# Kernel optimization log

Hardware: AMD Instinct MI355X
Metric: run time of the kernel (lower is better)

The kernel has to match this reference:

```python
import jax, jax.numpy as jnp
import numpy as np

T, IN_DIM, HID, OUT = 32768, 500, 300, 100


def setup_inputs() -> dict:
    key = jax.random.key(0)
    ks = jax.random.split(key, 12)
    s_in = 1.0 / np.sqrt(HID)
    inp = {
        'input_seq': jax.random.normal(ks[0], (T, IN_DIM), jnp.float32),
        'W_ih0': jax.random.uniform(ks[1], (HID, IN_DIM), jnp.float32, -s_in, s_in),
        'W_hh0': jax.random.uniform(ks[2], (HID, HID), jnp.float32, -s_in, s_in),
        'b_ih0': jax.random.uniform(ks[3], (HID,), jnp.float32, -s_in, s_in),
        'b_hh0': jax.random.uniform(ks[4], (HID,), jnp.float32, -s_in, s_in),
        'W_ih1': jax.random.uniform(ks[5], (HID, HID), jnp.float32, -s_in, s_in),
        'W_hh1': jax.random.uniform(ks[6], (HID, HID), jnp.float32, -s_in, s_in),
        'b_ih1': jax.random.uniform(ks[7], (HID,), jnp.float32, -s_in, s_in),
        'b_hh1': jax.random.uniform(ks[8], (HID,), jnp.float32, -s_in, s_in),
        'W_lin': jax.random.uniform(ks[9], (OUT, HID), jnp.float32, -s_in, s_in),
        'b_lin': jax.random.uniform(ks[10], (OUT,), jnp.float32, -s_in, s_in),
    }
    return inp


def _rnn_layer(x_proj, W_hh):
    # x_proj: [T, H] = precomputed input projection + both biases
    # h_t = tanh(x_proj_t + h_{t-1} @ W_hh^T), h_0 = 0 (PyTorch nn.RNN semantics)
    def step(h, xp):
        h_new = jnp.tanh(xp + h @ W_hh.T)
        return h_new, h_new
    h0 = jnp.zeros((W_hh.shape[0],), x_proj.dtype)
    _, hs = jax.lax.scan(step, h0, x_proj)
    return hs  # [T, H]


def reference(input_seq, W_ih0, W_hh0, b_ih0, b_hh0, W_ih1, W_hh1, b_ih1, b_hh1, W_lin, b_lin):
    # Layer 0: batch-1 vanilla tanh RNN; vectorize input GEMM over all timesteps
    x0 = input_seq @ W_ih0.T + (b_ih0 + b_hh0)  # [T, HID]
    h0 = _rnn_layer(x0, W_hh0)
    # Layer 1 consumes layer-0 hidden sequence
    x1 = h0 @ W_ih1.T + (b_ih1 + b_hh1)  # [T, HID]
    h1 = _rnn_layer(x1, W_hh1)
    # Linear head over flattened [T, HID]
    return h1 @ W_lin.T + b_lin  # [T, OUT]
```

## Files before the change

kernel.cpp:

```cpp
#include <hip/hip_runtime.h>
#include <cstddef>

#define T_LEN 32768
#define HID   300
#define HP    304
#define HK    320
#define KC    10
#define IN_D  500
#define OUT_D 100
#define OUTP  104
#define DIST  2
#define CHUNK 64
#define NCHUNK (T_LEN / CHUNK)

typedef _Float16 f16x8 __attribute__((ext_vector_type(8)));
typedef float    f32x4 __attribute__((ext_vector_type(4)));

__device__ __align__(16) float    g_x  [(size_t)(T_LEN + 8) * HP];
__device__ __align__(16) float    g_x1 [(size_t)(T_LEN + 8) * HP];
__device__ __align__(16) _Float16 g_h0h[(size_t)T_LEN * HP + 64];
__device__ __align__(16) _Float16 g_h1h[(size_t)T_LEN * HP + 64];
__device__ __align__(16) float    g_wt0[IN_D * HP];
__device__ __align__(16) float    g_wtl[HID * OUTP];
__device__ int g_flag0;
__device__ int g_flag1;

__global__ void k_reset() { g_flag0 = 0; g_flag1 = 0; }

__global__ void k_transpose(const float* __restrict__ src, int J, int K, int JP, int dst_sel)
{
    float* dst = (dst_sel == 0) ? g_wt0 : g_wtl;
    int idx = blockIdx.x * 256 + threadIdx.x;
    if (idx >= K * JP) return;
    int k = idx / JP, j = idx - k * JP;
    dst[idx] = (j < J) ? src[j * K + k] : 0.f;
}

__global__ __launch_bounds__(320) void k_gemm_in(const float* __restrict__ inp,
                                                 const float* __restrict__ b1,
                                                 const float* __restrict__ b2)
{
    __shared__ float lds[32 * IN_D];
    const int tid = threadIdx.x;
    const int t0  = blockIdx.x * 32;
    {
        const f32x4* src4 = (const f32x4*)(inp + (size_t)t0 * IN_D);
        f32x4* lds4 = (f32x4*)lds;
        const int n4 = (32 * IN_D) >> 2;
        for (int i = tid; i < n4; i += 320) lds4[i] = src4[i];
    }
    __syncthreads();
    const int j = tid;
    if (j >= HP) return;
    float acc[32];
#pragma unroll
    for (int i = 0; i < 32; i++) acc[i] = 0.f;
#pragma unroll 4
    for (int k = 0; k < IN_D; k++) {
        float w = g_wt0[k * HP + j];
#pragma unroll
        for (int i = 0; i < 32; i++) acc[i] += w * lds[i * IN_D + k];
    }
    const float bias = (j < HID) ? (b1[j] + b2[j]) : 0.f;
#pragma unroll 4
    for (int i = 0; i < 32; i++) g_x[(size_t)(t0 + i) * HP + j] = acc[i] + bias;
}

__global__ __launch_bounds__(128) void k_gemm_out(const float* __restrict__ blin,
                                                  float* __restrict__ out)
{
    __shared__ float lds[64 * HP];
    const int tid = threadIdx.x;
    const int t0  = blockIdx.x * 64;
    {
        const f16x8* src8 = (const f16x8*)(g_h1h + (size_t)t0 * HP);
        const int n8 = (64 * HP) / 8;
        for (int i = tid; i < n8; i += 128) {
            f16x8 v = src8[i];
            float* d = &lds[i * 8];
#pragma unroll
            for (int e = 0; e < 8; e++) d[e] = (float)v[e];
        }
    }
    __syncthreads();
    const int j = tid;
    if (j >= OUTP) return;
    float acc[64];
#pragma unroll
    for (int i = 0; i < 64; i++) acc[i] = 0.f;
#pragma unroll 2
    for (int k = 0; k < HID; k++) {
        float w = g_wtl[k * OUTP + j];
#pragma unroll
        for (int i = 0; i < 64; i++) acc[i] += w * lds[i * HP + k];
    }
    if (j < OUT_D) {
        float b = blin[j];
        for (int i = 0; i < 64; i++) out[(size_t)(t0 + i) * OUT_D + j] = acc[i] + b;
    }
}

__device__ __forceinline__ float fast_tanh(float v)
{
    float e = __expf(2.f * v);
    return 1.f - 2.f * __builtin_amdgcn_rcpf(e + 1.f);
}

__device__ __forceinline__ float sel4(f32x4 a, bool c1, bool c2)
{
    float v01 = c1 ? a[1] : a[0];
    float v23 = c1 ? a[3] : a[2];
    return c2 ? v23 : v01;
}

__device__ __forceinline__ f16x8 loadw_frag(const float* __restrict__ W,
                                            int tile, int col, int g, int kc)
{
    const int row = tile * 16 + col;
    const int kb  = kc * 32 + g * 8;
    f16x8 f;
#pragma unroll
    for (int j = 0; j < 8; j++) {
        const int k = kb + j;
        float wv = (row < HID && k < HID) ? W[row * HID + k] : 0.f;
        f[j] = (_Float16)wv;
    }
    return f;
}

__device__ __forceinline__ void wait_flag(int* f, int target)
{
    if (threadIdx.x == 0) {
        while (__hip_atomic_load(f, __ATOMIC_ACQUIRE, __HIP_MEMORY_SCOPE_AGENT) < target)
            __builtin_amdgcn_s_sleep(8);
    }
    __syncthreads();
}

__device__ __forceinline__ void publish_flag(int* f, int v)
{
    __syncthreads();
    if (threadIdx.x == 0)
        __hip_atomic_store(f, v, __ATOMIC_RELEASE, __HIP_MEMORY_SCOPE_AGENT);
}

#define MF(a_, b_, c_) __builtin_amdgcn_mfma_f32_16x16x32_f16((a_), (b_), (c_), 0, 0, 0)

template<int ROLE0>
__device__ __forceinline__ void scan_role(_Float16 (*hlds)[HK],
                                          const float* __restrict__ Whh,
                                          const float* __restrict__ xin,
                                          _Float16* __restrict__ hseq)
{
    const int tid  = threadIdx.x;
    const int lane = tid & 63;
    const int wave = tid >> 6;
    const int col  = lane & 15;
    const int g    = lane >> 4;
    const bool c1  = (col & 1) != 0;
    const bool c2  = (col & 2) != 0;
    const bool writer = (col < 4);

    const int tA = wave, tB = wave + 8, tC = wave + 16;
    const bool hasC = (wave < 3);
    const int wbA = tA * 16 + g * 4;
    const int wbB = tB * 16 + g * 4;
    const int wbC = tC * 16 + g * 4;

    for (int i = tid; i < 2 * HK; i += 512) ((_Float16*)hlds)[i] = (_Float16)0.f;

    f16x8 wA[KC], wB[KC], wC[KC];
#pragma unroll
    for (int kc = 0; kc < KC; kc++) {
        wA[kc] = loadw_frag(Whh, tA, col, g, kc);
        wB[kc] = loadw_frag(Whh, tB, col, g, kc);
        if (hasC) wC[kc] = loadw_frag(Whh, tC, col, g, kc);
        else {
            f16x8 z;
#pragma unroll
            for (int j = 0; j < 8; j++) z[j] = (_Float16)0.f;
            wC[kc] = z;
        }
    }

    __syncthreads();

    if (!ROLE0) wait_flag(&g_flag1, NCHUNK < 2 ? NCHUNK : 2);

    const f32x4 Z = {0.f, 0.f, 0.f, 0.f};

    f32x4 xA[DIST], xB[DIST], xC[DIST];
#pragma unroll
    for (int s = 0; s < DIST; s++) {
        xA[s] = *(const f32x4*)&xin[(size_t)s * HP + wbA];
        xB[s] = *(const f32x4*)&xin[(size_t)s * HP + wbB];
        xC[s] = hasC ? *(const f32x4*)&xin[(size_t)s * HP + wbC] : Z;
    }

#define STEP(t_, R_, s_) do {                                                          \
        f16x8 bf[KC];                                                                  \
        _Pragma("unroll")                                                              \
        for (int kc = 0; kc < KC; kc++)                                                \
            bf[kc] = *(const f16x8*)&hlds[R_][kc * 32 + g * 8];                        \
        f32x4 xvA = xA[s_], xvB = xB[s_], xvC = xC[s_];                                \
        xA[s_] = *(const f32x4*)&xin[(size_t)((t_) + DIST) * HP + wbA];                \
        xB[s_] = *(const f32x4*)&xin[(size_t)((t_) + DIST) * HP + wbB];                \
        if (hasC) xC[s_] = *(const f32x4*)&xin[(size_t)((t_) + DIST) * HP + wbC];      \
                                            \
        f32x4 cA0 = MF(wA[0], bf[0], xvA), cB0 = MF(wB[0], bf[0], xvB);                \
        f32x4 cC0 = hasC ? MF(wC[0], bf[0], xvC) : Z;                                  \
        f32x4 cA1 = MF(wA[3], bf[3], Z),   cB1 = MF(wB[3], bf[3], Z);                  \
        f32x4 cC1 = hasC ? MF(wC[3], bf[3], Z) : Z;                                    \
        f32x4 cA2 = MF(wA[6], bf[6], Z),   cB2 = MF(wB[6], bf[6], Z);                  \
        f32x4 cC2 = hasC ? MF(wC[6], bf[6], Z) : Z;                                    \
        f32x4 cA3 = MF(wA[8], bf[8], Z),   cB3 = MF(wB[8], bf[8], Z);                  \
        f32x4 cC3 = hasC ? MF(wC[8], bf[8], Z) : Z;                                    \
                                                                          \
        cA0 = MF(wA[1], bf[1], cA0); cB0 = MF(wB[1], bf[1], cB0);                      \
        if (hasC) cC0 = MF(wC[1], bf[1], cC0);                                         \
        cA1 = MF(wA[4], bf[4], cA1); cB1 = MF(wB[4], bf[4], cB1);                      \
        if (hasC) cC1 = MF(wC[4], bf[4], cC1);                                         \
        cA2 = MF(wA[7], bf[7], cA2); cB2 = MF(wB[7], bf[7], cB2);                      \
        if (hasC) cC2 = MF(wC[7], bf[7], cC2);                                         \
        cA3 = MF(wA[9], bf[9], cA3); cB3 = MF(wB[9], bf[9], cB3);                      \
        if (hasC) cC3 = MF(wC[9], bf[9], cC3);                                         \
                                                        \
        cA0 = MF(wA[2], bf[2], cA0); cB0 = MF(wB[2], bf[2], cB0);                      \
        if (hasC) cC0 = MF(wC[2], bf[2], cC0);                                         \
        cA1 = MF(wA[5], bf[5], cA1); cB1 = MF(wB[5], bf[5], cB1);                      \
        if (hasC) cC1 = MF(wC[5], bf[5], cC1);                                         \
                                                              \
        f32x4 sumA = (cA0 + cA1) + (cA2 + cA3);                                        \
        f32x4 sumB = (cB0 + cB1) + (cB2 + cB3);                                        \
        float yA = fast_tanh(sel4(sumA, c1, c2));                                      \
        float yB = fast_tanh(sel4(sumB, c1, c2));                                      \
        float yC = 0.f;                                                                \
        if (hasC) {                                                                    \
            f32x4 sumC = (cC0 + cC1) + (cC2 + cC3);                                    \
            yC = fast_tanh(sel4(sumC, c1, c2));                                        \
        }                                                                              \
        if (writer) {                                                                  \
            _Float16 hA = (_Float16)yA, hB = (_Float16)yB, hC = (_Float16)yC;          \
            hlds[1 - (R_)][wbA + col] = hA;                                            \
            hlds[1 - (R_)][wbB + col] = hB;                                            \
            if (hasC) hlds[1 - (R_)][wbC + col] = hC;                                  \
            hseq[(size_t)(t_) * HP + wbA + col] = hA;                                  \
            hseq[(size_t)(t_) * HP + wbB + col] = hB;                                  \
            if (hasC) hseq[(size_t)(t_) * HP + wbC + col] = hC;                        \
        }                                                                              \
    } while (0)

#define BAR() asm volatile("s_waitcnt lgkmcnt(0)\n\ts_barrier" ::: "memory")

#pragma unroll 1
    for (int c = 0; c < NCHUNK; ++c) {
        if (!ROLE0 && c > 0) {
            int tgt = (c + 2) < NCHUNK ? (c + 2) : NCHUNK;
            wait_flag(&g_flag1, tgt);
        }
#pragma unroll 1
        for (int tt = 0; tt < CHUNK; tt += 2) {
            const int tb = c * CHUNK + tt;
            STEP(tb + 0, 0, 0); BAR();
            STEP(tb + 1, 1, 1); BAR();
        }
        if (ROLE0) publish_flag(&g_flag0, c + 1);
    }
#undef STEP
#undef BAR
}

__device__ __forceinline__ void proj_role(const float* __restrict__ Wih,
                                          const float* __restrict__ b1,
                                          const float* __restrict__ b2)
{
    const int tid  = threadIdx.x;
    const int lane = tid & 63;
    const int wave = tid >> 6;
    const int col  = lane & 15;
    const int g    = lane >> 4;

    const int tA = wave, tB = wave + 8, tC = wave + 16;
    const bool hasC = (wave < 3);

    f16x8 wA[KC], wB[KC], wC[KC];
#pragma unroll
    for (int kc = 0; kc < KC; kc++) {
        wA[kc] = loadw_frag(Wih, tA, col, g, kc);
        wB[kc] = loadw_frag(Wih, tB, col, g, kc);
        if (hasC) wC[kc] = loadw_frag(Wih, tC, col, g, kc);
        else {
            f16x8 z;
#pragma unroll
            for (int j = 0; j < 8; j++) z[j] = (_Float16)0.f;
            wC[kc] = z;
        }
    }
    f32x4 bA, bB, bC;
#pragma unroll
    for (int e = 0; e < 4; e++) {
        int jA = tA * 16 + g * 4 + e, jB = tB * 16 + g * 4 + e, jC = tC * 16 + g * 4 + e;
        bA[e] = (jA < HID) ? b1[jA] + b2[jA] : 0.f;
        bB[e] = (jB < HID) ? b1[jB] + b2[jB] : 0.f;
        bC[e] = (hasC && jC < HID) ? b1[jC] + b2[jC] : 0.f;
    }

    const f32x4 zero4 = {0.f, 0.f, 0.f, 0.f};

#pragma unroll 1
    for (int c = 0; c < NCHUNK; ++c) {
        wait_flag(&g_flag0, c + 1);
        const int tbase = c * CHUNK;
#pragma unroll
        for (int tg = 0; tg < 4; ++tg) {
            const int t = tbase + tg * 16 + col;
            f16x8 bf[KC];
#pragma unroll
            for (int kc = 0; kc < KC; ++kc)
                bf[kc] = *(const f16x8*)&g_h0h[(size_t)t * HP + kc * 32 + g * 8];
            f32x4 aA = zero4, aB = zero4, aC = zero4;
#pragma unroll
            for (int kc = 0; kc < KC; ++kc) {
                aA = MF(wA[kc], bf[kc], aA);
                aB = MF(wB[kc], bf[kc], aB);
                if (hasC) aC = MF(wC[kc], bf[kc], aC);
            }
            *(f32x4*)&g_x1[(size_t)t * HP + tA * 16 + g * 4] = aA + bA;
            *(f32x4*)&g_x1[(size_t)t * HP + tB * 16 + g * 4] = aB + bB;
            if (hasC)
            *(f32x4*)&g_x1[(size_t)t * HP + tC * 16 + g * 4] = aC + bC;
        }
        publish_flag(&g_flag1, c + 1);
    }
}

__global__ __launch_bounds__(512, 2) void k_pipeline(const float* __restrict__ W_hh0,
                                                     const float* __restrict__ W_ih1,
                                                     const float* __restrict__ b_ih1,
                                                     const float* __restrict__ b_hh1,
                                                     const float* __restrict__ W_hh1)
{
    __shared__ __align__(16) _Float16 hlds[2][HK];
    if (blockIdx.x == 0)
        scan_role<1>(hlds, W_hh0, g_x, g_h0h);
    else if (blockIdx.x == 1)
        proj_role(W_ih1, b_ih1, b_hh1);
    else
        scan_role<0>(hlds, W_hh1, g_x1, g_h1h);
}

extern "C" void kernel_launch(void* const* d_in, const int* in_sizes, int n_in,
                              void* d_out, int out_size, void* d_ws, size_t ws_size,
                              hipStream_t stream)
{
    (void)in_sizes; (void)n_in; (void)d_ws; (void)ws_size; (void)out_size;
    const float* input = (const float*)d_in[0];
    const float* W_ih0 = (const float*)d_in[1];
    const float* W_hh0 = (const float*)d_in[2];
    const float* b_ih0 = (const float*)d_in[3];
    const float* b_hh0 = (const float*)d_in[4];
    const float* W_ih1 = (const float*)d_in[5];
    const float* W_hh1 = (const float*)d_in[6];
    const float* b_ih1 = (const float*)d_in[7];
    const float* b_hh1 = (const float*)d_in[8];
    const float* W_lin = (const float*)d_in[9];
    const float* b_lin = (const float*)d_in[10];
    float* out = (float*)d_out;

    k_reset<<<dim3(1), dim3(1), 0, stream>>>();
    k_transpose<<<dim3((IN_D * HP + 255) / 256), dim3(256), 0, stream>>>(W_ih0, HID, IN_D, HP, 0);
    k_transpose<<<dim3((HID * OUTP + 255) / 256), dim3(256), 0, stream>>>(W_lin, OUT_D, HID, OUTP, 2);

    k_gemm_in<<<dim3(T_LEN / 32), dim3(320), 0, stream>>>(input, b_ih0, b_hh0);

    k_pipeline<<<dim3(3), dim3(512), 0, stream>>>(W_hh0, W_ih1, b_ih1, b_hh1, W_hh1);

    k_gemm_out<<<dim3(T_LEN / 64), dim3(128), 0, stream>>>(b_lin, out);
}
```

Measured before the change: 26.04 ms.

## Spread recurrent scan over 12 waves with two tiles each and deeper prefetch

Raises the pipeline block from 8 to 12 waves, so each wave owns at most two 16-row output tiles of the 19 instead of three. This shortens the serial MFMA chain per timestep. Each lane now loads one scalar x value per tile, added after the MFMA reduction instead of being used as the accumulator init. The prefetch distance goes from 2 to 4 and the step loop is unrolled by 4. The trade-off is more waves joining each per-step barrier and higher block-level register pressure under the new launch bounds.

```diff
diff --git a/kernel.cpp b/kernel.cpp
--- a/kernel.cpp
+++ b/kernel.cpp
@@ -9,9 +9,10 @@
 #define IN_D  500
 #define OUT_D 100
 #define OUTP  104
-#define DIST  2
+#define DIST  4
 #define CHUNK 64
 #define NCHUNK (T_LEN / CHUNK)
+#define NWAVE 12
 
 typedef _Float16 f16x8 __attribute__((ext_vector_type(8)));
 typedef float    f32x4 __attribute__((ext_vector_type(4)));
@@ -157,29 +158,28 @@
     const int wave = tid >> 6;
     const int col  = lane & 15;
     const int g    = lane >> 4;
+    const int rr   = col & 3;
     const bool c1  = (col & 1) != 0;
     const bool c2  = (col & 2) != 0;
     const bool writer = (col < 4);
 
-    const int tA = wave, tB = wave + 8, tC = wave + 16;
-    const bool hasC = (wave < 3);
-    const int wbA = tA * 16 + g * 4;
-    const int wbB = tB * 16 + g * 4;
-    const int wbC = tC * 16 + g * 4;
-
-    for (int i = tid; i < 2 * HK; i += 512) ((_Float16*)hlds)[i] = (_Float16)0.f;
-
-    f16x8 wA[KC], wB[KC], wC[KC];
+    const int tA = wave, tB = wave + NWAVE;
+    const bool hasB = (wave < 7);
+    const int rowA = tA * 16 + g * 4 + rr;
+    const int rowB = tB * 16 + g * 4 + rr;
+
+    for (int i = tid; i < 2 * HK; i += 64 * NWAVE) ((_Float16*)hlds)[i] = (_Float16)0.f;
+
+    f16x8 wA[KC], wB[KC];
 #pragma unroll
     for (int kc = 0; kc < KC; kc++) {
         wA[kc] = loadw_frag(Whh, tA, col, g, kc);
-        wB[kc] = loadw_frag(Whh, tB, col, g, kc);
-        if (hasC) wC[kc] = loadw_frag(Whh, tC, col, g, kc);
+        if (hasB) wB[kc] = loadw_frag(Whh, tB, col, g, kc);
         else {
             f16x8 z;
 #pragma unroll
             for (int j = 0; j < 8; j++) z[j] = (_Float16)0.f;
-            wC[kc] = z;
+            wB[kc] = z;
         }
     }
 
@@ -187,66 +187,47 @@
 
     if (!ROLE0) wait_flag(&g_flag1, NCHUNK < 2 ? NCHUNK : 2);
 
+    float xA[DIST], xB[DIST];
+#pragma unroll
+    for (int s = 0; s < DIST; s++) {
+        xA[s] = xin[(size_t)s * HP + rowA];
+        xB[s] = hasB ? xin[(size_t)s * HP + rowB] : 0.f;
+    }
+
     const f32x4 Z = {0.f, 0.f, 0.f, 0.f};
-
-    f32x4 xA[DIST], xB[DIST], xC[DIST];
-#pragma unroll
-    for (int s = 0; s < DIST; s++) {
-        xA[s] = *(const f32x4*)&xin[(size_t)s * HP + wbA];
-        xB[s] = *(const f32x4*)&xin[(size_t)s * HP + wbB];
-        xC[s] = hasC ? *(const f32x4*)&xin[(size_t)s * HP + wbC] : Z;
-    }
 
 #define STEP(t_, R_, s_) do {                                                          \
         f16x8 bf[KC];                                                                  \
         _Pragma("unroll")                                                              \
         for (int kc = 0; kc < KC; kc++)                                                \
             bf[kc] = *(const f16x8*)&hlds[R_][kc * 32 + g * 8];                        \
-        f32x4 xvA = xA[s_], xvB = xB[s_], xvC = xC[s_];                                \
-        xA[s_] = *(const f32x4*)&xin[(size_t)((t_) + DIST) * HP + wbA];                \
-        xB[s_] = *(const f32x4*)&xin[(size_t)((t_) + DIST) * HP + wbB];                \
-        if (hasC) xC[s_] = *(const f32x4*)&xin[(size_t)((t_) + DIST) * HP + wbC];      \
-                                            \
-        f32x4 cA0 = MF(wA[0], bf[0], xvA), cB0 = MF(wB[0], bf[0], xvB);                \
-        f32x4 cC0 = hasC ? MF(wC[0], bf[0], xvC) : Z;                                  \
-        f32x4 cA1 = MF(wA[3], bf[3], Z),   cB1 = MF(wB[3], bf[3], Z);                  \
-        f32x4 cC1 = hasC ? MF(wC[3], bf[3], Z) : Z;                                    \
-        f32x4 cA2 = MF(wA[6], bf[6], Z),   cB2 = MF(wB[6], bf[6], Z);                  \
-        f32x4 cC2 = hasC ? MF(wC[6], bf[6], Z) : Z;                                    \
-        f32x4 cA3 = MF(wA[8], bf[8], Z),   cB3 = MF(wB[8], bf[8], Z);                  \
-        f32x4 cC3 = hasC ? MF(wC[8], bf[8], Z) : Z;                                    \
-                                                                          \
-        cA0 = MF(wA[1], bf[1], cA0); cB0 = MF(wB[1], bf[1], cB0);                      \
-        if (hasC) cC0 = MF(wC[1], bf[1], cC0);                                         \
-        cA1 = MF(wA[4], bf[4], cA1); cB1 = MF(wB[4], bf[4], cB1);                      \
-        if (hasC) cC1 = MF(wC[4], bf[4], cC1);                                         \
-        cA2 = MF(wA[7], bf[7], cA2); cB2 = MF(wB[7], bf[7], cB2);                      \
-        if (hasC) cC2 = MF(wC[7], bf[7], cC2);                                         \
-        cA3 = MF(wA[9], bf[9], cA3); cB3 = MF(wB[9], bf[9], cB3);                      \
-        if (hasC) cC3 = MF(wC[9], bf[9], cC3);                                         \
-                                                        \
-        cA0 = MF(wA[2], bf[2], cA0); cB0 = MF(wB[2], bf[2], cB0);                      \
-        if (hasC) cC0 = MF(wC[2], bf[2], cC0);                                         \
-        cA1 = MF(wA[5], bf[5], cA1); cB1 = MF(wB[5], bf[5], cB1);                      \
-        if (hasC) cC1 = MF(wC[5], bf[5], cC1);                                         \
-                                                              \
-        f32x4 sumA = (cA0 + cA1) + (cA2 + cA3);                                        \
-        f32x4 sumB = (cB0 + cB1) + (cB2 + cB3);                                        \
-        float yA = fast_tanh(sel4(sumA, c1, c2));                                      \
-        float yB = fast_tanh(sel4(sumB, c1, c2));                                      \
-        float yC = 0.f;                                                                \
-        if (hasC) {                                                                    \
-            f32x4 sumC = (cC0 + cC1) + (cC2 + cC3);                                    \
-            yC = fast_tanh(sel4(sumC, c1, c2));                                        \
+        float xvA = xA[s_], xvB = xB[s_];                                              \
+        xA[s_] = xin[(size_t)((t_) + DIST) * HP + rowA];                               \
+        if (hasB) xB[s_] = xin[(size_t)((t_) + DIST) * HP + rowB];                     \
+        f32x4 aA0 = MF(wA[0], bf[0], Z);                                               \
+        f32x4 aB0 = hasB ? MF(wB[0], bf[0], Z) : Z;                                    \
+        f32x4 aA1 = MF(wA[5], bf[5], Z);                                               \
+        f32x4 aB1 = hasB ? MF(wB[5], bf[5], Z) : Z;                                    \
+        _Pragma("unroll")                                                              \
+        for (int j = 1; j < 5; j++) {                                                  \
+            aA0 = MF(wA[j], bf[j], aA0);                                               \
+            if (hasB) aB0 = MF(wB[j], bf[j], aB0);                                     \
+            aA1 = MF(wA[j + 5], bf[j + 5], aA1);                                       \
+            if (hasB) aB1 = MF(wB[j + 5], bf[j + 5], aB1);                             \
+        }                                                                              \
+        float sA = sel4(aA0, c1, c2) + sel4(aA1, c1, c2);                              \
+        float yA = fast_tanh(sA + xvA);                                                \
+        float yB = 0.f;                                                                \
+        if (hasB) {                                                                    \
+            float sB = sel4(aB0, c1, c2) + sel4(aB1, c1, c2);                          \
+            yB = fast_tanh(sB + xvB);                                                  \
         }                                                                              \
         if (writer) {                                                                  \
-            _Float16 hA = (_Float16)yA, hB = (_Float16)yB, hC = (_Float16)yC;          \
-            hlds[1 - (R_)][wbA + col] = hA;                                            \
-            hlds[1 - (R_)][wbB + col] = hB;                                            \
-            if (hasC) hlds[1 - (R_)][wbC + col] = hC;                                  \
-            hseq[(size_t)(t_) * HP + wbA + col] = hA;                                  \
-            hseq[(size_t)(t_) * HP + wbB + col] = hB;                                  \
-            if (hasC) hseq[(size_t)(t_) * HP + wbC + col] = hC;                        \
+            _Float16 hA = (_Float16)yA, hB = (_Float16)yB;                             \
+            hlds[1 - (R_)][tA * 16 + g * 4 + col] = hA;                                \
+            if (hasB) hlds[1 - (R_)][tB * 16 + g * 4 + col] = hB;                      \
+            hseq[(size_t)(t_) * HP + rowA] = hA;                                       \
+            if (hasB) hseq[(size_t)(t_) * HP + rowB] = hB;                             \
         }                                                                              \
     } while (0)
 
@@ -259,10 +240,12 @@
             wait_flag(&g_flag1, tgt);
         }
 #pragma unroll 1
-        for (int tt = 0; tt < CHUNK; tt += 2) {
+        for (int tt = 0; tt < CHUNK; tt += DIST) {
             const int tb = c * CHUNK + tt;
             STEP(tb + 0, 0, 0); BAR();
             STEP(tb + 1, 1, 1); BAR();
+            STEP(tb + 2, 0, 2); BAR();
+            STEP(tb + 3, 1, 3); BAR();
         }
         if (ROLE0) publish_flag(&g_flag0, c + 1);
     }
@@ -280,29 +263,27 @@
     const int col  = lane & 15;
     const int g    = lane >> 4;
 
-    const int tA = wave, tB = wave + 8, tC = wave + 16;
-    const bool hasC = (wave < 3);
-
-    f16x8 wA[KC], wB[KC], wC[KC];
+    const int tA = wave, tB = wave + NWAVE;
+    const bool hasB = (wave < 7);
+
+    f16x8 wA[KC], wB[KC];
 #pragma unroll
     for (int kc = 0; kc < KC; kc++) {
         wA[kc] = loadw_frag(Wih, tA, col, g, kc);
-        wB[kc] = loadw_frag(Wih, tB, col, g, kc);
-        if (hasC) wC[kc] = loadw_frag(Wih, tC, col, g, kc);
+        if (hasB) wB[kc] = loadw_frag(Wih, tB, col, g, kc);
         else {
             f16x8 z;
 #pragma unroll
             for (int j = 0; j < 8; j++) z[j] = (_Float16)0.f;
-            wC[kc] = z;
-        }
-    }
-    f32x4 bA, bB, bC;
+            wB[kc] = z;
+        }
+    }
+    f32x4 bA, bB;
 #pragma unroll
     for (int e = 0; e < 4; e++) {
-        int jA = tA * 16 + g * 4 + e, jB = tB * 16 + g * 4 + e, jC = tC * 16 + g * 4 + e;
+        int jA = tA * 16 + g * 4 + e, jB = tB * 16 + g * 4 + e;
         bA[e] = (jA < HID) ? b1[jA] + b2[jA] : 0.f;
-        bB[e] = (jB < HID) ? b1[jB] + b2[jB] : 0.f;
-        bC[e] = (hasC && jC < HID) ? b1[jC] + b2[jC] : 0.f;
+        bB[e] = (hasB && jB < HID) ? b1[jB] + b2[jB] : 0.f;
     }
 
     const f32x4 zero4 = {0.f, 0.f, 0.f, 0.f};
@@ -318,27 +299,25 @@
 #pragma unroll
             for (int kc = 0; kc < KC; ++kc)
                 bf[kc] = *(const f16x8*)&g_h0h[(size_t)t * HP + kc * 32 + g * 8];
-            f32x4 aA = zero4, aB = zero4, aC = zero4;
+            f32x4 aA = zero4, aB = zero4;
 #pragma unroll
             for (int kc = 0; kc < KC; ++kc) {
                 aA = MF(wA[kc], bf[kc], aA);
-                aB = MF(wB[kc], bf[kc], aB);
-                if (hasC) aC = MF(wC[kc], bf[kc], aC);
+                if (hasB) aB = MF(wB[kc], bf[kc], aB);
             }
             *(f32x4*)&g_x1[(size_t)t * HP + tA * 16 + g * 4] = aA + bA;
+            if (hasB)
             *(f32x4*)&g_x1[(size_t)t * HP + tB * 16 + g * 4] = aB + bB;
-            if (hasC)
-            *(f32x4*)&g_x1[(size_t)t * HP + tC * 16 + g * 4] = aC + bC;
         }
         publish_flag(&g_flag1, c + 1);
     }
 }
 
-__global__ __launch_bounds__(512, 2) void k_pipeline(const float* __restrict__ W_hh0,
-                                                     const float* __restrict__ W_ih1,
-                                                     const float* __restrict__ b_ih1,
-                                                     const float* __restrict__ b_hh1,
-                                                     const float* __restrict__ W_hh1)
+__global__ __launch_bounds__(64 * NWAVE, 3) void k_pipeline(const float* __restrict__ W_hh0,
+                                                            const float* __restrict__ W_ih1,
+                                                            const float* __restrict__ b_ih1,
+                                                            const float* __restrict__ b_hh1,
+                                                            const float* __restrict__ W_hh1)
 {
     __shared__ __align__(16) _Float16 hlds[2][HK];
     if (blockIdx.x == 0)
@@ -373,7 +352,7 @@
 
     k_gemm_in<<<dim3(T_LEN / 32), dim3(320), 0, stream>>>(input, b_ih0, b_hh0);
 
-    k_pipeline<<<dim3(3), dim3(512), 0, stream>>>(W_hh0, W_ih1, b_ih1, b_hh1, W_hh1);
+    k_pipeline<<<dim3(3), dim3(64 * NWAVE), 0, stream>>>(W_hh0, W_ih1, b_ih1, b_hh1, W_hh1);
 
     k_gemm_out<<<dim3(T_LEN / 64), dim3(128), 0, stream>>>(b_lin, out);
 }
```

Result: faster. 22.69 ms (-12.9%).
